# Performance work log

Hardware: AMD Instinct MI355X
Metric: run time of the kernel (lower is better)

Reference implementation:

```python
import jax, jax.numpy as jnp
import numpy as np
import math

H = 512        # hidden_dim
DEPTH = 5
KS = 3         # kernel size
DELTA = 0.1
M = 104        # timestamp == seq_len
NC = 5
B = 512
BN_EPS = 1e-5


def setup_inputs() -> dict:
    key = jax.random.key(0)
    ks = jax.random.split(key, 16)
    inp = {}
    inp['x'] = jax.random.normal(ks[0], (B, 1, M), dtype=jnp.float32)
    # CausalCNN: depth conv layers (first is 1->H, rest H->H), each followed by BN
    inp['conv_w0'] = jax.random.normal(ks[1], (H, 1, KS), dtype=jnp.float32) * (1.0 / np.sqrt(KS))
    inp['conv_b0'] = jnp.zeros((H,), jnp.float32)
    inp['conv_w'] = jax.random.normal(ks[2], (DEPTH - 1, H, H, KS), dtype=jnp.float32) * (1.0 / np.sqrt(H * KS))
    inp['conv_b'] = jnp.zeros((DEPTH - 1, H), jnp.float32)
    inp['bn_gamma'] = jnp.ones((DEPTH, H), jnp.float32)
    inp['bn_beta'] = jnp.zeros((DEPTH, H), jnp.float32)
    # input_proj
    inp['proj_w'] = jax.random.normal(ks[3], (H, H), dtype=jnp.float32) * (1.0 / np.sqrt(H))
    inp['proj_b'] = jnp.zeros((H,), jnp.float32)
    # ZOH layers: A = -0.01*I + 0.001*randn, B = 0.01*randn [H,1], C = 0.01*randn [1,H]
    eye = jnp.eye(H, dtype=jnp.float32)
    inp['A_all'] = -0.01 * eye[None] + 0.001 * jax.random.normal(ks[4], (DEPTH, H, H), dtype=jnp.float32)
    inp['B_all'] = 0.01 * jax.random.normal(ks[5], (DEPTH, H, 1), dtype=jnp.float32)
    inp['C_all'] = 0.01 * jax.random.normal(ks[6], (DEPTH, 1, H), dtype=jnp.float32)
    # fc_temp: Linear(H,H) -> BN1d(H) -> GELU -> Dropout(eval) -> Linear(H,NC)
    inp['fc1_w'] = jax.random.normal(ks[7], (H, H), dtype=jnp.float32) * (1.0 / np.sqrt(H))
    inp['fc1_b'] = jnp.zeros((H,), jnp.float32)
    inp['fc_bn_gamma'] = jnp.ones((H,), jnp.float32)
    inp['fc_bn_beta'] = jnp.zeros((H,), jnp.float32)
    inp['fc2_w'] = jax.random.normal(ks[8], (NC, H), dtype=jnp.float32) * (1.0 / np.sqrt(H))
    inp['fc2_b'] = jnp.zeros((NC,), jnp.float32)
    return inp


def _causal_conv(x, w, b):
    # x: [B, Cin, T], w: [Cout, Cin, K] -> left-pad K-1 (equivalent to pad both + trim right)
    y = jax.lax.conv_general_dilated(x, w, window_strides=(1,), padding=[(KS - 1, 0)],
                                     dimension_numbers=('NCH', 'OIH', 'NCH'))
    return y + b[None, :, None]


def _bn_ct(x, g, b):
    # BatchNorm1d over [B, C, T], batch statistics (training-mode normalization)
    m = x.mean(axis=(0, 2), keepdims=True)
    v = x.var(axis=(0, 2), keepdims=True)
    return g[None, :, None] * (x - m) * jax.lax.rsqrt(v + BN_EPS) + b[None, :, None]


def _pos_encoding(T, d):
    pos = jnp.arange(T, dtype=jnp.float32)[:, None]
    div = jnp.exp(jnp.arange(0, d, 2, dtype=jnp.float32) * (-math.log(10000.0) / d))
    pe = jnp.zeros((T, d), jnp.float32)
    pe = pe.at[:, 0::2].set(jnp.sin(pos * div))
    pe = pe.at[:, 1::2].set(jnp.cos(pos * div))
    return pe


def _zoh_kbar(A, Bv, Cv):
    # A: [H,H], Bv: [H,1], Cv: [1,H] -> normalized K_bar [M]
    A_bar = jax.scipy.linalg.expm(DELTA * A)
    I = jnp.eye(H, dtype=A.dtype)
    A_inv = jnp.linalg.inv(A + 0.001 * I)
    B_bar = A_inv @ (A_bar - I) @ (DELTA * Bv)  # [H,1]
    # term_k = C @ A_bar^k @ B_bar; sequential vector recurrence replaces matrix powers
    def step(v, _):
        term = (Cv @ v)[0, 0]
        return A_bar @ v, term
    _, terms = jax.lax.scan(step, B_bar, None, length=M)  # [M]
    Kb = jnp.flip(terms, axis=0)
    return Kb / (jnp.linalg.norm(Kb) + 1e-6)


def reference(x, conv_w0, conv_b0, conv_w, conv_b, bn_gamma, bn_beta, proj_w, proj_b,
              A_all, B_all, C_all, fc1_w, fc1_b, fc_bn_gamma, fc_bn_beta, fc2_w, fc2_b):
    # CausalCNN
    h = jax.nn.relu(_bn_ct(_causal_conv(x, conv_w0, conv_b0), bn_gamma[0], bn_beta[0]))
    for i in range(DEPTH - 1):
        h = jax.nn.relu(_bn_ct(_causal_conv(h, conv_w[i], conv_b[i]), bn_gamma[i + 1], bn_beta[i + 1]))
    h = jnp.transpose(h, (0, 2, 1))  # [B, T, H]
    # positional encoding + input projection
    h = h + _pos_encoding(M, H)[None]
    h = jnp.einsum('bth,oh->bto', h, proj_w) + proj_b
    # stacked ZOH kernels: each layer multiplies x by its normalized K_bar along time
    Ks = jax.vmap(_zoh_kbar)(A_all, B_all, C_all)  # [DEPTH, M]
    h = h * jnp.prod(Ks, axis=0)[None, :, None]
    # mean pool over time, then fc_temp (BN with batch stats, dropout = identity/eval)
    h = h.mean(axis=1)  # [B, H]
    h = jnp.dot(h, fc1_w.T) + fc1_b
    m = h.mean(axis=0, keepdims=True)
    v = h.var(axis=0, keepdims=True)
    h = fc_bn_gamma * (h - m) * jax.lax.rsqrt(v + BN_EPS) + fc_bn_beta
    h = jax.nn.gelu(h, approximate=False)
    logits = jnp.dot(h, fc2_w.T) + fc2_b  # [B, NC]
    return logits
```

## Files before the change

kernel.cpp:

```cpp
#include <hip/hip_runtime.h>
#include <cstdio>
#include <cmath>
#include <cstdint>

constexpr int BM = 512 * 104;
constexpr float BN_EPS = 1e-5f;

constexpr size_t SZ_BF   = (size_t)BM * 512 * 2;
constexpr size_t SZ_MAT5 = (size_t)5 * 512 * 512 * 4;
constexpr size_t OFF_YB0 = 0;
constexpr size_t OFF_YB1 = OFF_YB0 + SZ_BF;
constexpr size_t OFF_WT2 = OFF_YB1 + SZ_BF;
constexpr size_t OFF_X   = OFF_WT2 + 6291456;
constexpr size_t OFF_T1  = OFF_X   + SZ_MAT5;
constexpr size_t OFF_T2  = OFF_T1  + SZ_MAT5;
constexpr size_t OFF_E   = OFF_T2  + SZ_MAT5;
constexpr size_t OFF_MW  = OFF_E   + SZ_MAT5;
constexpr size_t OFF_P2  = OFF_MW  + SZ_MAT5;
constexpr size_t OFF_P4  = OFF_P2  + SZ_MAT5;
constexpr size_t OFF_ROWT= OFF_P4  + SZ_MAT5;
constexpr size_t OFF_COLS= OFF_ROWT + 655360;
constexpr size_t OFF_COLS2=OFF_COLS + 655360;
constexpr size_t OFF_PIVI= OFF_COLS2 + 655360;
constexpr size_t OFF_PJT = OFF_PIVI + 81920;
// ... 7 lines not shown
constexpr size_t OFF_V   = OFF_SV  + 10240;
constexpr size_t OFF_WV  = OFF_V   + 81920;
constexpr size_t OFF_S   = OFF_WV  + 133120;
constexpr size_t WS_NEED = OFF_S + 512;

__device__ __forceinline__ float bf2f(unsigned short u) {
    union { uint32_t i; float f; } x; x.i = (uint32_t)u << 16; return x.f;
}
__device__ __forceinline__ unsigned short f2bf(float f) {
    union { float f; uint32_t i; } x; x.f = f;
    uint32_t r = x.i + 0x7FFFu + ((x.i >> 16) & 1u);
    return (unsigned short)(r >> 16);
}

typedef __bf16 bf16x8 __attribute__((ext_vector_type(8)));
typedef float  f32x4  __attribute__((ext_vector_type(4)));

__device__ __forceinline__ void gld16(const void* g, void* l) {
    __builtin_amdgcn_global_load_lds((const __attribute__((address_space(1))) uint32_t*)g,
                                     (__attribute__((address_space(3))) uint32_t*)l, 16, 0, 0);
}

__device__ __forceinline__ uint32_t bnrelu_pk(uint32_t u, float sc0, float sc1, float sh0, float sh1) {
    union { uint32_t i; float f; } a, b;
    a.i = u << 16;
    b.i = u & 0xFFFF0000u;
    float x0 = fmaxf(fmaf(a.f, sc0, sh0), 0.0f);
    float x1 = fmaxf(fmaf(b.f, sc1, sh1), 0.0f);
    uint32_t r;
    asm volatile("v_cvt_pk_bf16_f32 %0, %1, %2" : "=v"(r) : "v"(x0), "v"(x1));
    return r;
}

__global__ void k_bw(const float* __restrict__ W, unsigned short* __restrict__ Wt2,
                     const float* __restrict__ Aall, float* __restrict__ X, float* __restrict__ MW,
                     float* __restrict__ COLSa, const float* __restrict__ Call, float* __restrict__ WV)
{
    int bid = blockIdx.x;
    int tid = threadIdx.x;
    if (bid < 2048) {
        int co = bid & 511, l = bid >> 9;
        const float* src = W + (long)(l * 512 + co) * 512 * 3;
        unsigned short* dst = Wt2 + (long)l * 3 * 262144 + ((long)co << 9);
        int v = (co >> 1) & 3;
#pragma unroll
        for (int q = 0; q < 2; ++q) {
            int ci = tid * 2 + q;
            int chunk = (ci >> 3) & 3;
            int di = (ci & ~31) + (((chunk ^ v) & 3) << 3) + (ci & 7);
            float f0 = src[ci * 3 + 0], f1 = src[ci * 3 + 1], f2 = src[ci * 3 + 2];
            dst[di] = f2bf(f0);
            dst[262144 + di] = f2bf(f1);
            dst[524288 + di] = f2bf(f2);
        }
        return;
    }
    long i = (long)(bid - 2048) * 256 + tid;
    float a = Aall[i];
    X[i] = 0.1f * a;
    int z = (int)(i >> 18);
    int rc = (int)(i & 262143);
    int r = rc >> 9, c = rc & 511;
    float mw = a + ((r == c) ? 0.001f : 0.0f);
    MW[i] = mw;
    if (c < 64) COLSa[(long)z * 32768 + r * 64 + c] = mw;
    if (i < 2560) WV[(i >> 9) * 6656 + (i & 511)] = Call[i];
}

__global__ __launch_bounds__(256) void k_mm(
    const float* __restrict__ A, long sA, int lda,
    const float* __restrict__ Bm, long sB, int ldb,
    float* __restrict__ C, long sC, int ldc,
    int K, int mode,
    const float* __restrict__ aux, long sAux,
    const float* __restrict__ aux2, float* __restrict__ Cp,
    double* __restrict__ st1, double* __restrict__ st2, int pc)
{
    __shared__ float sm[2 * 32 * 68];
    float* As = sm;
    float* Bs = sm + 32 * 68;
    int z = blockIdx.z;
    A  += (long)z * sA;
    Bm += (long)z * sB;
    C  += (long)z * sC;
    if (aux) aux += (long)z * sAux;
    int m0 = blockIdx.x * 64, n0 = blockIdx.y * 64;
    int tid = threadIdx.x;
    int tx = tid & 15, ty = tid >> 4;
    float acc[4][4] = {};
    for (int k0 = 0; k0 < K; k0 += 32) {
        __syncthreads();
#pragma unroll
        for (int it = 0; it < 2; ++it) {
            int s = it * 256 + tid;
            int mm = s >> 3, k4 = (s & 7) * 4;
            float4 v = *(const float4*)&A[(long)(m0 + mm) * lda + k0 + k4];
            As[(k4 + 0) * 68 + mm] = v.x;
            As[(k4 + 1) * 68 + mm] = v.y;
            As[(k4 + 2) * 68 + mm] = v.z;
// ... 45 lines not shown
                int col = col0 + j;
                pv[j] = ((row == col) ? 0.5f : 0.0f) + aux[(long)row * 512 + col] * (1.0f / 6.0f)
                        + v[j] * (1.0f / 24.0f);
            }
            *(float4*)&Cp[base] = make_float4(pv[0], pv[1], pv[2], pv[3]);
        } else if (mode == 8) {
            for (int j = 0; j < 4; ++j) {
                v[j] += aux[col0 + j];
                cs1[j] += v[j]; cs2[j] += v[j] * v[j];
            }
        }
        *(float4*)&C[base] = make_float4(v[0], v[1], v[2], v[3]);
    }
    if (mode == 8) {
        __syncthreads();
        float* s1s = sm;
        float* s2s = sm + 1024;
#pragma unroll
        for (int j = 0; j < 4; ++j) {
            s1s[ty * 64 + tx * 4 + j] = cs1[j];
            s2s[ty * 64 + tx * 4 + j] = cs2[j];
        }
        __syncthreads();
        if (tid < 64) {
            double a = 0.0, b = 0.0;
#pragma unroll
            for (int t = 0; t < 16; ++t) { a += s1s[t * 64 + tid]; b += s2s[t * 64 + tid]; }
            atomicAdd(&st1[n0 + tid], a);
            atomicAdd(&st2[n0 + tid], b);
        }
    }
}

__global__ __launch_bounds__(256) void k_elim2(
    const float* __restrict__ MWin, float* __restrict__ MWout,
    const float* __restrict__ PIVI, const float* __restrict__ COLSc,
    float* __restrict__ COLSn, int pc, int pcn)
{
    __shared__ float As[64 * 68];
    __shared__ float Rs[64 * 68];
    int z = blockIdx.z;
    MWin += (long)z * 262144; MWout += (long)z * 262144;
    PIVI += z * 4096; COLSc += (long)z * 32768; COLSn += (long)z * 32768;
    int m0 = blockIdx.x * 64, n0 = blockIdx.y * 64;
    int tid = threadIdx.x;
    int tx = tid & 15, ty = tid >> 4;

    if (n0 == pc) {
        for (int it = 0; it < 16; ++it) {
            int idx = it * 256 + tid;
            int r = idx >> 6, c = idx & 63;
            Rs[r * 68 + c] = PIVI[r * 64 + c];
        }
        __syncthreads();
    } else {
        {
            int m = tid >> 2, kb = (tid & 3) * 16;
#pragma unroll
            for (int u = 0; u < 4; ++u) {
                float4 v = *(const float4*)&PIVI[m * 64 + kb + u * 4];
                As[(kb + u * 4 + 0) * 68 + m] = v.x;
                As[(kb + u * 4 + 1) * 68 + m] = v.y;
                As[(kb + u * 4 + 2) * 68 + m] = v.z;
                As[(kb + u * 4 + 3) * 68 + m] = v.w;
            }
            int kr = tid >> 2, cb = (tid & 3) * 16;
#pragma unroll
            for (int u = 0; u < 4; ++u)
                *(float4*)&Rs[kr * 68 + cb + u * 4] =
                    *(const float4*)&MWin[(long)(pc + kr) * 512 + n0 + cb + u * 4];
        }
        __syncthreads();
        float acc1[4][4] = {};
// ... 24 lines not shown
            int r = idx >> 6, c = idx & 63;
            float v = Rs[r * 68 + c];
            MWout[(long)(pc + r) * 512 + n0 + c] = v;
            if (n0 == pcn) COLSn[(pc + r) * 64 + c] = v;
        }
        return;
    }
    {
        int m = tid >> 2, kb = (tid & 3) * 16;
#pragma unroll
        for (int u = 0; u < 4; ++u) {
            float4 v = *(const float4*)&COLSc[(m0 + m) * 64 + kb + u * 4];
            As[(kb + u * 4 + 0) * 68 + m] = v.x;
            As[(kb + u * 4 + 1) * 68 + m] = v.y;
            As[(kb + u * 4 + 2) * 68 + m] = v.z;
            As[(kb + u * 4 + 3) * 68 + m] = v.w;
        }
    }
    __syncthreads();
    float acc[4][4] = {};
#pragma unroll 8
    for (int kk = 0; kk < 64; ++kk) {
        float4 a = *(const float4*)&As[kk * 68 + ty * 4];
        float4 b = *(const float4*)&Rs[kk * 68 + tx * 4];
        float av[4] = {a.x, a.y, a.z, a.w};
        float bv[4] = {b.x, b.y, b.z, b.w};
#pragma unroll
        for (int i = 0; i < 4; ++i)
#pragma unroll
            for (int j = 0; j < 4; ++j)
                acc[i][j] = fmaf(av[i], bv[j], acc[i][j]);
    }
    bool inP = (n0 == pc);
#pragma unroll
    for (int i = 0; i < 4; ++i) {
        int row = m0 + ty * 4 + i;
        int col0 = n0 + tx * 4;
        long base = (long)row * 512 + col0;
        float ov[4] = {0.f, 0.f, 0.f, 0.f};
        if (!inP) {
            float4 oldv = *(const float4*)&MWin[base];
            ov[0] = oldv.x; ov[1] = oldv.y; ov[2] = oldv.z; ov[3] = oldv.w;
        }
        float v[4];
#pragma unroll
        for (int j = 0; j < 4; ++j) v[j] = ov[j] - acc[i][j];
        *(float4*)&MWout[base] = make_float4(v[0], v[1], v[2], v[3]);
        if (n0 == pcn)
            *(float4*)&COLSn[row * 64 + (col0 - pcn)] = make_float4(v[0], v[1], v[2], v[3]);
    }
}

__global__ __launch_bounds__(256) void k_inv64(const float* __restrict__ MW, int pblk, float* __restrict__ PIVI)
{
    __shared__ float mat[64 * 65];
    __shared__ float fv[64];
    __shared__ int perm[64];
    __shared__ int arr[64];
    __shared__ int pividx;
    __shared__ float dv;
    int z = blockIdx.x;
    const float* Mg = MW + (long)z * 262144 + (long)pblk * 64 * 512 + pblk * 64;
    int tid = threadIdx.x;
    for (int it = 0; it < 16; ++it) {
        int idx = it * 256 + tid;
        int r = idx >> 6, c = idx & 63;
        mat[r * 65 + c] = Mg[r * 512 + c];
    }
    __syncthreads();
    for (int j = 0; j < 64; ++j) {
        if (tid < 64) {
            float v = (tid >= j) ? fabsf(mat[tid * 65 + j]) : -1.0f;
            int idx = tid;
#pragma unroll
            for (int off = 32; off; off >>= 1) {
                float ov = __shfl_down(v, off);
                int oi = __shfl_down(idx, off);
                if (ov > v) { v = ov; idx = oi; }
            }
            if (tid == 0) pividx = idx;
        }
        __syncthreads();
// ... 13 lines not shown
            mat[j * 65 + tid] = (tid == j) ? d : mat[j * 65 + tid] * d;
            if (tid == 0) dv = d;
        }
        __syncthreads();
        {
            int i = tid & 63, c0 = (tid >> 6) * 16;
            if (i != j) {
                float f = fv[i];
                float dd = dv;
#pragma unroll
                for (int u = 0; u < 16; ++u) {
                    int c = c0 + u;
                    float val = mat[i * 65 + c] - f * mat[j * 65 + c];
                    if (c == j) val = -f * dd;
                    mat[i * 65 + c] = val;
                }
            }
        }
        __syncthreads();
    }
    if (tid == 0) {
        for (int c = 0; c < 64; ++c) arr[c] = c;
        for (int j = 63; j >= 0; --j) { int r = perm[j]; int t = arr[j]; arr[j] = arr[r]; arr[r] = t; }
    }
    __syncthreads();
    float* Pg = PIVI + z * 4096;
    for (int it = 0; it < 16; ++it) {
        int idx = it * 256 + tid;
        int r = idx >> 6, c = idx & 63;
        Pg[r * 64 + c] = mat[r * 65 + arr[c]];
    }
}

__global__ __launch_bounds__(1024) void k_bbar(const float* __restrict__ Eb, const float* __restrict__ MW,
                                               const float* __restrict__ Aall, const float* __restrict__ Ball,
                                               float* __restrict__ V)
{
    __shared__ float xs[512], us[512], vs[512], sv[512];
    int z = blockIdx.x;
    const float* E  = Eb   + (long)z * 262144;
    const float* Mi = MW   + (long)z * 262144;
    const float* Aa = Aall + (long)z * 262144;
    int tid = threadIdx.x, lane = tid & 63, w = tid >> 6;
    if (tid < 512) xs[tid] = Ball[z * 512 + tid];
    __syncthreads();
    for (int r = w * 32; r < w * 32 + 32; ++r) {
        const float* ar = E + (long)r * 512;
        double acc = 0.0;
#pragma unroll
        for (int m = 0; m < 8; ++m) acc += (double)ar[lane + m * 64] * (double)xs[lane + m * 64];
        for (int off = 32; off; off >>= 1) acc += __shfl_down(acc, off);
        if (lane == 0) us[r] = 0.1f * (float)acc;
    }
    __syncthreads();
    for (int r = w * 32; r < w * 32 + 32; ++r) {
        const float* ar = Mi + (long)r * 512;
        double acc = 0.0;
#pragma unroll
        for (int m = 0; m < 8; ++m) acc += (double)ar[lane + m * 64] * (double)us[lane + m * 64];
        for (int off = 32; off; off >>= 1) acc += __shfl_down(acc, off);
        if (lane == 0) vs[r] = 1.0f * (float)acc;
    }
    __syncthreads();
    for (int r = w * 32; r < w * 32 + 32; ++r) {
        const float* ar = Aa + (long)r * 512;
        double acc = 0.0;
#pragma unroll
        for (int m = 0; m < 8; ++m) acc += (double)ar[lane + m * 64] * (double)vs[lane + m * 64];
        for (int off = 32; off; off >>= 1) acc += __shfl_down(acc, off);
        if (lane == 0) {
            float val = 1.0f * (float)acc + 0.001f * vs[r];
            sv[r] = us[r] - val;
        }
    }
    __syncthreads();
    for (int r = w * 32; r < w * 32 + 32; ++r) {
        const float* ar = Mi + (long)r * 512;
        double acc = 0.0;
#pragma unroll
        for (int m = 0; m < 8; ++m) acc += (double)ar[lane + m * 64] * (double)sv[lane + m * 64];
        for (int off = 32; off; off >>= 1) acc += __shfl_down(acc, off);
        if (lane == 0) V[(long)z * 4096 + r] = vs[r] + 1.0f * (float)acc;
    }
}

struct VWT { long a[8]; long x[8]; long y[8]; float al[8]; float be[8]; int ty[8]; };
__global__ void k_vw(const char* __restrict__ ws, VWT T)
{
    int g = blockIdx.x, z = blockIdx.y, t = blockIdx.z;
    int lane = threadIdx.x;
    const float* A = (const float*)(ws + T.a[t]) + (long)z * 262144;
    int ty = T.ty[t];
    long vs = ty ? 6656 : 4096;
    const float* x = (const float*)(ws + T.x[t]) + (long)z * vs;
    float* yv = (float*)(ws + T.y[t]) + (long)z * vs;
    if (ty == 0) {
        float xm[8];
#pragma unroll
        for (int m = 0; m < 8; ++m) xm[m] = x[lane + m * 64];
        float alpha = T.al[t], beta = T.be[t];
        for (int r0 = 0; r0 < 64; ++r0) {
            int row = g * 64 + r0;
            const float* ar = A + (long)row * 512;
            double acc = 0.0;
#pragma unroll
            for (int m = 0; m < 8; ++m) acc += (double)ar[lane + m * 64] * (double)xm[m];
            for (int off = 32; off; off >>= 1) acc += __shfl_down(acc, off);
            if (lane == 0) yv[row] = alpha * (float)acc + beta * x[row];
        }
    } else {
        __shared__ float xl[512];
#pragma unroll
        for (int m = 0; m < 8; ++m) xl[lane + m * 64] = x[lane + m * 64];
        __syncthreads();
        int c = g * 64 + lane;
        double acc = 0.0;
#pragma unroll 8
        for (int j = 0; j < 512; ++j) acc += (double)A[(long)j * 512 + c] * (double)xl[j];
        yv[c] = (float)acc;
    }
}

__global__ __launch_bounds__(512) void k_termsk(const float* __restrict__ WV, const float* __restrict__ V,
                                                float* __restrict__ svec)
{
    __shared__ float tl[520];
    __shared__ float invn[5];
    __shared__ float red[2];
    int tid = threadIdx.x;
    for (int t = tid; t < 520; t += 512) {
        int z = t / 104, d = t - z * 104;
        int j = d >> 3, i = d & 7;
        const float* wp = WV + z * 6656 + j * 512;
        const float* vp = V + z * 4096 + i * 512;
        float acc = 0.0f;
#pragma unroll 8
        for (int k = 0; k < 512; ++k) acc += wp[k] * vp[k];
        tl[t] = acc;
    }
    __syncthreads();
    int w = tid >> 6, lane = tid & 63;
    if (w < 5) {
        float a = tl[w * 104 + lane]; a = a * a;
        if (lane < 40) { float b = tl[w * 104 + 64 + lane]; a += b * b; }
#pragma unroll
        for (int off = 32; off; off >>= 1) a += __shfl_down(a, off);
        if (lane == 0) invn[w] = 1.0f / (sqrtf(a) + 1e-6f);
    }
    __syncthreads();
    float s = 0.0f;
    if (tid < 104) {
        s = 1.0f;
        for (int l = 0; l < 5; ++l) s *= tl[l * 104 + (103 - tid)] * invn[l];
        svec[tid] = s;
    }
    if (tid < 128) {
        float v = (tid < 104) ? s : 0.0f;
#pragma unroll
        for (int off = 32; off; off >>= 1) v += __shfl_down(v, off);
        if ((tid & 63) == 0) red[tid >> 6] = v;
    }
    __syncthreads();
    if (tid == 0) svec[104] = (red[0] + red[1]) * (1.0f / 104.0f);
}

__global__ void k_conv0(const float* __restrict__ x, const float* __restrict__ w0, const float* __restrict__ b0,
                        unsigned short* __restrict__ y, double* __restrict__ s1g, double* __restrict__ s2g)
{
    int b = blockIdx.x;
    int c = blockIdx.y * 256 + threadIdx.x;
    float w_0 = w0[c * 3 + 0], w_1 = w0[c * 3 + 1], w_2 = w0[c * 3 + 2], bb = b0[c];
    const float* xb = x + b * 104;
    unsigned short* yb = y + (long)b * 104 * 512 + c;
    float xm2 = 0.0f, xm1 = 0.0f;
    float s1 = 0.0f, s2 = 0.0f;
    for (int t = 0; t < 104; ++t) {
        float x0 = xb[t];
        float v = w_0 * xm2 + w_1 * xm1 + w_2 * x0 + bb;
        yb[t * 512] = f2bf(v);
        s1 += v; s2 += v * v;
        xm2 = xm1; xm1 = x0;
    }
    atomicAdd(&s1g[c], (double)s1);
    atomicAdd(&s2g[c], (double)s2);
}

__global__ __launch_bounds__(256, 2) void k_convm(
    const unsigned short* __restrict__ act,
    const unsigned short* __restrict__ Wt2,
    const float* __restrict__ bias,
    const double* __restrict__ STin,
    const float* __restrict__ gam, const float* __restrict__ bet,
    unsigned short* __restrict__ yout,
    double* __restrict__ s1g, double* __restrict__ s2g)
{
    __shared__ __align__(16) unsigned short As[130 * 32];
    __shared__ __align__(16) unsigned short Bs[3 * 256 * 32];
    __shared__ float SCs[512];
    __shared__ float SHs[512];
    int tid = threadIdx.x;
    int m0 = blockIdx.x * 128, co0 = blockIdx.y * 256;
    int w = tid >> 6, lane = tid & 63;
    int wr = (w >> 1) * 64, wc = (w & 1) * 128;
    int fr = lane & 15, quad = lane >> 4;

    const double invN = 1.0 / (double)BM;
    for (int c = tid; c < 512; c += 256) {
        double mn = STin[c] * invN;
        double var = STin[512 + c] * invN - mn * mn;
        double rs = 1.0 / sqrt(var + (double)BN_EPS);
        double scd = (double)gam[c] * rs;
        SCs[c] = (float)scd;
        SHs[c] = (float)((double)bet[c] - mn * scd);
    }

    bool valid[4][3];
#pragma unroll
    for (int i = 0; i < 4; ++i) {
        int R = m0 + wr + i * 16 + fr;
        int t = R % 104;
#pragma unroll
        for (int tau = 0; tau < 3; ++tau) valid[i][tau] = (t + tau >= 2);
    }

    int aoff[4][3];
#pragma unroll
    for (int i = 0; i < 4; ++i)
#pragma unroll
        for (int tau = 0; tau < 3; ++tau) {
            int r = wr + i * 16 + fr + tau;
            aoff[i][tau] = r * 32 + (((quad ^ (r >> 1)) & 3) << 3);
        }
    int boff[8];
// ... 118 lines not shown
        float b = st[512 + half * 128 + cl] + st[512 + (half + 2) * 128 + cl];
        atomicAdd(&s1g[co0 + tid], (double)a);
        atomicAdd(&s2g[co0 + tid], (double)b);
    }
}

__global__ void k_pool(const unsigned short* __restrict__ y4, const double* __restrict__ ST4,
                       const float* __restrict__ gam, const float* __restrict__ bet,
                       const float* __restrict__ svec, float* __restrict__ g)
{
    __shared__ float sl[104];
    int b = blockIdx.x;
    int c = blockIdx.y * 256 + threadIdx.x;
    if (threadIdx.x < 104) sl[threadIdx.x] = svec[threadIdx.x];
    __syncthreads();
    const double invN = 1.0 / (double)BM;
    double mn = ST4[c] * invN;
    double var = ST4[512 + c] * invN - mn * mn;
    double rs = 1.0 / sqrt(var + (double)BN_EPS);
    double scd = (double)gam[c] * rs;
    float sc = (float)scd, sh = (float)((double)bet[c] - mn * scd);
    int he = c & ~1;
    float div = expf((float)he * (-0.017988946039015984f));
    float acc = 0.0f;
    const unsigned short* yb = y4 + (long)b * 104 * 512 + c;
    for (int t = 0; t < 104; ++t) {
        float v = bf2f(yb[t * 512]);
        float hn = fmaxf(fmaf(v, sc, sh), 0.0f);
        float arg = (float)t * div;
        float pe = (c & 1) ? cosf(arg) : sinf(arg);
        acc += sl[t] * (hn + pe);
    }
    g[(long)b * 512 + c] = acc * (1.0f / 104.0f);
}

__global__ void k_t512(const float* __restrict__ in0, float* __restrict__ out0,
                       const float* __restrict__ in1, float* __restrict__ out1)
{
    __shared__ float tile[64 * 68];
    const float* in = blockIdx.z ? in1 : in0;
    float* outp = blockIdx.z ? out1 : out0;
    int bx = blockIdx.x, by = blockIdx.y;
    int tid = threadIdx.x;
    for (int it = 0; it < 4; ++it) {
        int s = it * 256 + tid;
        int r = s >> 4, c4 = (s & 15) * 4;
        *(float4*)&tile[r * 68 + c4] = *(const float4*)&in[(long)(bx * 64 + r) * 512 + by * 64 + c4];
    }
    __syncthreads();
    for (int it = 0; it < 4; ++it) {
        int s = it * 256 + tid;
        int r = s >> 4, c4 = (s & 15) * 4;
        float4 v;
        v.x = tile[(c4 + 0) * 68 + r];
        v.y = tile[(c4 + 1) * 68 + r];
        v.z = tile[(c4 + 2) * 68 + r];
        v.w = tile[(c4 + 3) * 68 + r];
        *(float4*)&outp[(long)(by * 64 + r) * 512 + bx * 64 + c4] = v;
    }
}

__global__ __launch_bounds__(256) void k_final(const float* __restrict__ zin, const double* __restrict__ st,
                                               const float* __restrict__ gam, const float* __restrict__ bet,
                                               const float* __restrict__ w2, const float* __restrict__ b2,
                                               float* __restrict__ outp)
{
    __shared__ float red[256];
    int b = blockIdx.x, tid = threadIdx.x;
    int oo[2] = { tid, tid + 256 };
    float gv[2];
#pragma unroll
    for (int q = 0; q < 2; ++q) {
        int o = oo[q];
        double m = st[o] * (1.0 / 512.0);
        double var = st[512 + o] * (1.0 / 512.0) - m * m;
        double rs = 1.0 / sqrt(var + (double)BN_EPS);
        float xn = (float)(((double)zin[(long)b * 512 + o] - m) * rs * (double)gam[o] + (double)bet[o]);
        gv[q] = 0.5f * xn * (1.0f + erff(xn * 0.70710678118654752f));
    }
    for (int n = 0; n < 5; ++n) {
        float p = gv[0] * w2[n * 512 + oo[0]] + gv[1] * w2[n * 512 + oo[1]];
        red[tid] = p;
        __syncthreads();
        for (int off = 128; off; off >>= 1) { if (tid < off) red[tid] += red[tid + off]; __syncthreads(); }
        if (tid == 0) outp[b * 5 + n] = red[0] + b2[n];
        __syncthreads();
    }
}

static void mm(hipStream_t s, int Mt, int Nt, int z,
               const float* A, long sA, int lda,
               const float* B, long sB, int ldb,
// ... 15 lines not shown
    const float* conv_w0 = (const float*)d_in[1];
    const float* conv_b0 = (const float*)d_in[2];
    const float* conv_w  = (const float*)d_in[3];
    const float* conv_b  = (const float*)d_in[4];
    const float* bn_g    = (const float*)d_in[5];
    const float* bn_b    = (const float*)d_in[6];
    const float* proj_w  = (const float*)d_in[7];
    const float* proj_b  = (const float*)d_in[8];
    const float* A_all   = (const float*)d_in[9];
    const float* B_all   = (const float*)d_in[10];
    const float* C_all   = (const float*)d_in[11];
    const float* fc1_w   = (const float*)d_in[12];
    const float* fc1_b   = (const float*)d_in[13];
    const float* fbn_g   = (const float*)d_in[14];
    const float* fbn_b   = (const float*)d_in[15];
    const float* fc2_w   = (const float*)d_in[16];
    const float* fc2_b   = (const float*)d_in[17];
    float* outp = (float*)d_out;
    char* ws = (char*)d_ws;
    if (ws_size < WS_NEED) { printf("ws too small: %zu < %zu\n", ws_size, WS_NEED); return; }

    unsigned short* YB0 = (unsigned short*)(ws + OFF_YB0);
    unsigned short* YB1 = (unsigned short*)(ws + OFF_YB1);
    unsigned short* WT2 = (unsigned short*)(ws + OFF_WT2);
    float* Xb   = (float*)(ws + OFF_X);
    float* T1   = (float*)(ws + OFF_T1);
    float* T2   = (float*)(ws + OFF_T2);
    float* Eb   = (float*)(ws + OFF_E);
    float* MW   = (float*)(ws + OFF_MW);
    float* P2   = (float*)(ws + OFF_P2);
    float* P4   = (float*)(ws + OFF_P4);
    float* COLS1= (float*)(ws + OFF_COLS);
    float* COLS2= (float*)(ws + OFF_COLS2);
    float* PIVI = (float*)(ws + OFF_PIVI);
    float* PJT  = (float*)(ws + OFF_PJT);
    float* F1T  = (float*)(ws + OFF_F1T);
    float* G    = (float*)(ws + OFF_G);
    float* POOL = (float*)(ws + OFF_POOL);
    float* Zb   = (float*)(ws + OFF_Z);
    double* ST  = (double*)(ws + OFF_ST);
    float* V    = (float*)(ws + OFF_V);
    float* WV   = (float*)(ws + OFF_WV);
    float* SVEC = (float*)(ws + OFF_S);

    const long SM = 262144;
    hipMemsetAsync(ws + OFF_ST, 0, 49152, stream);

    k_bw<<<7168, 256, 0, stream>>>(conv_w, WT2, A_all, Xb, MW, COLS1, C_all, WV);

    {
        float* MB[2] = { MW, P2 };
        for (int p = 0; p < 8; ++p) {
            int pc = p * 64;
            float* Mi = MB[p & 1];
            float* Mo = MB[(p + 1) & 1];
            float* Cc = (p & 1) ? COLS2 : COLS1;
            float* Cn = (p & 1) ? COLS1 : COLS2;
            k_inv64<<<5, 256, 0, stream>>>(Mi, p, PIVI);
            k_elim2<<<dim3(8, 8, 5), 256, 0, stream>>>(Mi, Mo, PIVI, Cc, Cn, pc, pc + 64);
        }
    }
    mm(stream, 8, 8, 5, Xb, SM, 512, Xb, SM, 512, T2, SM, 512, 512, 7, Xb, SM, nullptr, T1);
    mm(stream, 8, 8, 5, T2, SM, 512, T1, SM, 512, Eb, SM, 512, 512, 2, Xb, SM);
    mm(stream, 8, 8, 5, Eb, SM, 512, Eb, SM, 512, Xb, SM, 512, 512, 1, Eb, SM);
    mm(stream, 8, 8, 5, Xb, SM, 512, Xb, SM, 512, T1, SM, 512, 512, 0);
    mm(stream, 8, 8, 5, T1, SM, 512, T1, SM, 512, T2, SM, 512, 512, 0);
    mm(stream, 8, 8, 5, T2, SM, 512, T2, SM, 512, P2, SM, 512, 512, 0);
    mm(stream, 8, 8, 5, P2, SM, 512, P2, SM, 512, P4, SM, 512, 512, 0);
    k_bbar<<<5, 1024, 0, stream>>>(Eb, MW, A_all, B_all, V);
    auto Voff = [](int i) { return (long)(OFF_V + (size_t)i * 2048); };
    auto Woff = [](int j) { return (long)(OFF_WV + (size_t)j * 2048); };
    {
        VWT T = {};
        T.a[0] = OFF_E;  T.x[0] = Voff(0); T.y[0] = Voff(1); T.al[0] = 1; T.be[0] = 1; T.ty[0] = 0;
        T.a[1] = OFF_T2; T.x[1] = Woff(0); T.y[1] = Woff(1); T.ty[1] = 1;
        k_vw<<<dim3(8, 5, 2), 64, 0, stream>>>(ws, T);
    }
    {
        VWT T = {};
        T.a[0] = OFF_X;  T.x[0] = Voff(0); T.y[0] = Voff(2); T.al[0] = 1; T.ty[0] = 0;
        T.a[1] = OFF_X;  T.x[1] = Voff(1); T.y[1] = Voff(3); T.al[1] = 1; T.ty[1] = 0;
        T.a[2] = OFF_P2; T.x[2] = Woff(0); T.y[2] = Woff(2); T.ty[2] = 1;
        T.a[3] = OFF_P2; T.x[3] = Woff(1); T.y[3] = Woff(3); T.ty[3] = 1;
        k_vw<<<dim3(8, 5, 4), 64, 0, stream>>>(ws, T);
    }
    {
        VWT T = {};
        for (int i = 0; i < 4; ++i) {
            T.a[i] = OFF_T1; T.x[i] = Voff(i); T.y[i] = Voff(4 + i); T.al[i] = 1; T.ty[i] = 0;
            T.a[4 + i] = OFF_P4; T.x[4 + i] = Woff(i); T.y[4 + i] = Woff(4 + i); T.ty[4 + i] = 1;
        }
        k_vw<<<dim3(8, 5, 8), 64, 0, stream>>>(ws, T);
    }
    {
        VWT T = {};
        for (int i = 0; i < 4; ++i) {
            T.a[i] = OFF_P4; T.x[i] = Woff(4 + i); T.y[i] = Woff(8 + i); T.ty[i] = 1;
        }
        k_vw<<<dim3(8, 5, 4), 64, 0, stream>>>(ws, T);
    }
    {
        VWT T = {};
        T.a[0] = OFF_P4; T.x[0] = Woff(8); T.y[0] = Woff(12); T.ty[0] = 1;
        k_vw<<<dim3(8, 5, 1), 64, 0, stream>>>(ws, T);
    }
    k_termsk<<<1, 512, 0, stream>>>(WV, V, SVEC);

    k_conv0<<<dim3(512, 2), 256, 0, stream>>>(x, conv_w0, conv_b0, YB0, ST, ST + 512);
    for (int l = 1; l <= 4; ++l) {
        unsigned short* inb  = (l & 1) ? YB0 : YB1;
        unsigned short* outb = (l & 1) ? YB1 : YB0;
        k_convm<<<dim3(416, 2), 256, 0, stream>>>(inb, WT2 + (size_t)(l - 1) * 3 * 262144,
                                                  conv_b + (l - 1) * 512,
                                                  ST + (l - 1) * 1024, bn_g + (l - 1) * 512, bn_b + (l - 1) * 512,
                                                  outb, ST + l * 1024, ST + l * 1024 + 512);
    }
    k_pool<<<dim3(512, 2), 256, 0, stream>>>(YB0, ST + 4 * 1024, bn_g + 4 * 512, bn_b + 4 * 512, SVEC, G);

    k_t512<<<dim3(8, 8, 2), 256, 0, stream>>>(proj_w, PJT, fc1_w, F1T);
    mm(stream, 8, 8, 1, G, 0, 512, PJT, 0, 512, POOL, 0, 512, 512, 5, proj_b, 0, SVEC + 104);
    mm(stream, 8, 8, 1, POOL, 0, 512, F1T, 0, 512, Zb, 0, 512, 512, 8, fc1_b, 0, nullptr, nullptr,
       ST + 5 * 1024, ST + 5 * 1024 + 512);
    k_final<<<512, 256, 0, stream>>>(Zb, ST + 5 * 1024, fbn_g, fbn_b, fc2_w, fc2_b, outp);
}
```

Before: 1.834 ms.

## Fuse small launches: pre-pass, pivot inversion into elimination, ZOH vector chain

Several small kernels are merged. The weight transposes and the first conv layer now run inside one pre-pass kernel. The 64x64 pivot-block inversion for the next step is folded into the elimination kernel, so only one block per batch does it. The chain of matrix-vector kernels plus k_bbar becomes one k_zoh kernel, and the k_termsk reduction rides on an extra block of the first conv layer. The goal is to cut launch overhead and serial small-kernel gaps. In exchange, the work is concentrated in a few blocks: the inversion tail of the elimination and five 1024-thread ZOH blocks, which may serialize.

```diff
diff --git a/kernel.cpp b/kernel.cpp
--- a/kernel.cpp
+++ b/kernel.cpp
@@ -63,10 +63,16 @@
     return r;
 }
 
-__global__ void k_bw(const float* __restrict__ W, unsigned short* __restrict__ Wt2,
-                     const float* __restrict__ Aall, float* __restrict__ X, float* __restrict__ MW,
-                     float* __restrict__ COLSa, const float* __restrict__ Call, float* __restrict__ WV)
+__global__ void k_pre(const float* __restrict__ W, unsigned short* __restrict__ Wt2,
+                      const float* __restrict__ Aall, float* __restrict__ X, float* __restrict__ MW,
+                      float* __restrict__ COLSa, const float* __restrict__ Call, float* __restrict__ WV,
+                      const float* __restrict__ pin0, float* __restrict__ pout0,
+                      const float* __restrict__ pin1, float* __restrict__ pout1,
+                      const float* __restrict__ xin, const float* __restrict__ w0,
+                      const float* __restrict__ b0, unsigned short* __restrict__ y0,
+                      double* __restrict__ s1g, double* __restrict__ s2g)
 {
+    __shared__ float tile[64 * 68];
     int bid = blockIdx.x;
     int tid = threadIdx.x;
     if (bid < 2048) {
@@ -86,16 +92,61 @@
         }
         return;
     }
-    long i = (long)(bid - 2048) * 256 + tid;
-    float a = Aall[i];
-    X[i] = 0.1f * a;
-    int z = (int)(i >> 18);
-    int rc = (int)(i & 262143);
-    int r = rc >> 9, c = rc & 511;
-    float mw = a + ((r == c) ? 0.001f : 0.0f);
-    MW[i] = mw;
-    if (c < 64) COLSa[(long)z * 32768 + r * 64 + c] = mw;
-    if (i < 2560) WV[(i >> 9) * 6656 + (i & 511)] = Call[i];
+    if (bid < 7168) {
+        long i = (long)(bid - 2048) * 256 + tid;
+        float a = Aall[i];
+        X[i] = 0.1f * a;
+        int z = (int)(i >> 18);
+        int rc = (int)(i & 262143);
+        int r = rc >> 9, c = rc & 511;
+        float mw = a + ((r == c) ? 0.001f : 0.0f);
+        MW[i] = mw;
+        if (c < 64) COLSa[(long)z * 32768 + r * 64 + c] = mw;
+        if (i < 2560) WV[(i >> 9) * 6656 + (i & 511)] = Call[i];
+        return;
+    }
+    if (bid < 7296) {
+        int id = bid - 7168;
+        int bx = id & 7, by = (id >> 3) & 7, zi = id >> 6;
+        const float* in = zi ? pin1 : pin0;
+        float* outp = zi ? pout1 : pout0;
+        for (int it = 0; it < 4; ++it) {
+            int s = it * 256 + tid;
+            int r = s >> 4, c4 = (s & 15) * 4;
+            *(float4*)&tile[r * 68 + c4] = *(const float4*)&in[(long)(bx * 64 + r) * 512 + by * 64 + c4];
+        }
+        __syncthreads();
+        for (int it = 0; it < 4; ++it) {
+            int s = it * 256 + tid;
+            int r = s >> 4, c4 = (s & 15) * 4;
+            float4 v;
+            v.x = tile[(c4 + 0) * 68 + r];
+            v.y = tile[(c4 + 1) * 68 + r];
+            v.z = tile[(c4 + 2) * 68 + r];
+            v.w = tile[(c4 + 3) * 68 + r];
+            *(float4*)&outp[(long)(by * 64 + r) * 512 + bx * 64 + c4] = v;
+        }
+        return;
+    }
+    {
+        int id = bid - 7296;
+        int b = id & 511;
+        int c = (id >> 9) * 256 + tid;
+        float w_0 = w0[c * 3 + 0], w_1 = w0[c * 3 + 1], w_2 = w0[c * 3 + 2], bb = b0[c];
+        const float* xb = xin + b * 104;
+        unsigned short* yb = y0 + (long)b * 104 * 512 + c;
+        float xm2 = 0.0f, xm1 = 0.0f;
+        float s1 = 0.0f, s2 = 0.0f;
+        for (int t = 0; t < 104; ++t) {
+            float x0 = xb[t];
+            float v = w_0 * xm2 + w_1 * xm1 + w_2 * x0 + bb;
+            yb[t * 512] = f2bf(v);
+            s1 += v; s2 += v * v;
+            xm2 = xm1; xm1 = x0;
+        }
+        atomicAdd(&s1g[c], (double)s1);
+        atomicAdd(&s2g[c], (double)s2);
+    }
 }
 
 __global__ __launch_bounds__(256) void k_mm(
@@ -207,13 +258,18 @@
     }
 }
 
-__global__ __launch_bounds__(256) void k_elim2(
+__global__ __launch_bounds__(256) void k_elim3(
     const float* __restrict__ MWin, float* __restrict__ MWout,
-    const float* __restrict__ PIVI, const float* __restrict__ COLSc,
-    float* __restrict__ COLSn, int pc, int pcn)
+    const float* __restrict__ PIVI, float* __restrict__ PIVN,
+    const float* __restrict__ COLSc, float* __restrict__ COLSn, int pc, int pcn)
 {
     __shared__ float As[64 * 68];
     __shared__ float Rs[64 * 68];
+    __shared__ float fv[64];
+    __shared__ int perm[64];
+    __shared__ int arr[64];
+    __shared__ int pividx;
+    __shared__ float dv;
     int z = blockIdx.z;
     MWin += (long)z * 262144; MWout += (long)z * 262144;
     PIVI += z * 4096; COLSc += (long)z * 32768; COLSn += (long)z * 32768;
@@ -304,6 +360,7 @@
                 acc[i][j] = fmaf(av[i], bv[j], acc[i][j]);
     }
     bool inP = (n0 == pc);
+    float vsav[4][4];
 #pragma unroll
     for (int i = 0; i < 4; ++i) {
         int row = m0 + ty * 4 + i;
@@ -316,10 +373,77 @@
         }
         float v[4];
 #pragma unroll
-        for (int j = 0; j < 4; ++j) v[j] = ov[j] - acc[i][j];
+        for (int j = 0; j < 4; ++j) { v[j] = ov[j] - acc[i][j]; vsav[i][j] = v[j]; }
         *(float4*)&MWout[base] = make_float4(v[0], v[1], v[2], v[3]);
         if (n0 == pcn)
             *(float4*)&COLSn[row * 64 + (col0 - pcn)] = make_float4(v[0], v[1], v[2], v[3]);
+    }
+
+    if (!(m0 == pcn && n0 == pcn)) return;
+    __syncthreads();
+    float* mat = As;
+#pragma unroll
+    for (int i = 0; i < 4; ++i)
+#pragma unroll
+        for (int j = 0; j < 4; ++j)
+            mat[(ty * 4 + i) * 65 + tx * 4 + j] = vsav[i][j];
+    __syncthreads();
+    for (int j = 0; j < 64; ++j) {
+        if (tid < 64) {
+            float v = (tid >= j) ? fabsf(mat[tid * 65 + j]) : -1.0f;
+            int idx = tid;
+#pragma unroll
+            for (int off = 32; off; off >>= 1) {
+                float ov = __shfl_down(v, off);
+                int oi = __shfl_down(idx, off);
+                if (ov > v) { v = ov; idx = oi; }
+            }
+            if (tid == 0) pividx = idx;
+        }
+        __syncthreads();
+        int r = pividx;
+        if (tid < 64) {
+            if (r != j) {
+                float tj = mat[j * 65 + tid], tr = mat[r * 65 + tid];
+                mat[j * 65 + tid] = tr; mat[r * 65 + tid] = tj;
+            }
+            if (tid == 0) perm[j] = r;
+        }
+        __syncthreads();
+        if (tid < 64) {
+            float piv = mat[j * 65 + j];
+            float d = 1.0f / piv;
+            fv[tid] = mat[tid * 65 + j];
+            mat[j * 65 + tid] = (tid == j) ? d : mat[j * 65 + tid] * d;
+            if (tid == 0) dv = d;
+        }
+        __syncthreads();
+        {
+            int i = tid & 63, c0 = (tid >> 6) * 16;
+            if (i != j) {
+                float f = fv[i];
+                float dd = dv;
+#pragma unroll
+                for (int u = 0; u < 16; ++u) {
+                    int c = c0 + u;
+                    float val = mat[i * 65 + c] - f * mat[j * 65 + c];
+                    if (c == j) val = -f * dd;
+                    mat[i * 65 + c] = val;
+                }
+            }
+        }
+        __syncthreads();
+    }
+    if (tid == 0) {
+        for (int c = 0; c < 64; ++c) arr[c] = c;
+        for (int j = 63; j >= 0; --j) { int r = perm[j]; int t = arr[j]; arr[j] = arr[r]; arr[r] = t; }
+    }
+    __syncthreads();
+    float* Pg = PIVN + z * 4096;
+    for (int it = 0; it < 16; ++it) {
+        int idx = it * 256 + tid;
+        int r = idx >> 6, c = idx & 63;
+        Pg[r * 64 + c] = mat[r * 65 + arr[c]];
     }
 }
 
@@ -399,17 +523,26 @@
     }
 }
 
-__global__ __launch_bounds__(1024) void k_bbar(const float* __restrict__ Eb, const float* __restrict__ MW,
-                                               const float* __restrict__ Aall, const float* __restrict__ Ball,
-                                               float* __restrict__ V)
+__global__ __launch_bounds__(1024) void k_zoh(const char* __restrict__ ws,
+                                              const float* __restrict__ Aall,
+                                              const float* __restrict__ Ball)
 {
-    __shared__ float xs[512], us[512], vs[512], sv[512];
+    __shared__ float Vs[8][512];
+    __shared__ float Ws[13][512];
+    __shared__ float xs[512], us[512], sv[512];
     int z = blockIdx.x;
-    const float* E  = Eb   + (long)z * 262144;
-    const float* Mi = MW   + (long)z * 262144;
-    const float* Aa = Aall + (long)z * 262144;
+    const float* E   = (const float*)(ws + OFF_E)  + (long)z * 262144;
+    const float* A2p = (const float*)(ws + OFF_X)  + (long)z * 262144;
+    const float* A4p = (const float*)(ws + OFF_T1) + (long)z * 262144;
+    const float* A8p = (const float*)(ws + OFF_T2) + (long)z * 262144;
+    const float* A16p= (const float*)(ws + OFF_P2) + (long)z * 262144;
+    const float* A32p= (const float*)(ws + OFF_P4) + (long)z * 262144;
+    const float* Mi  = (const float*)(ws + OFF_MW) + (long)z * 262144;
+    const float* Aa  = Aall + (long)z * 262144;
+    float* Vg = (float*)(ws + OFF_V)  + (long)z * 4096;
+    float* Wg = (float*)(ws + OFF_WV) + (long)z * 6656;
     int tid = threadIdx.x, lane = tid & 63, w = tid >> 6;
-    if (tid < 512) xs[tid] = Ball[z * 512 + tid];
+    if (tid < 512) { xs[tid] = Ball[z * 512 + tid]; Ws[0][tid] = Wg[tid]; }
     __syncthreads();
     for (int r = w * 32; r < w * 32 + 32; ++r) {
         const float* ar = E + (long)r * 512;
@@ -426,17 +559,17 @@
 #pragma unroll
         for (int m = 0; m < 8; ++m) acc += (double)ar[lane + m * 64] * (double)us[lane + m * 64];
         for (int off = 32; off; off >>= 1) acc += __shfl_down(acc, off);
-        if (lane == 0) vs[r] = 1.0f * (float)acc;
+        if (lane == 0) Vs[0][r] = 1.0f * (float)acc;
     }
     __syncthreads();
     for (int r = w * 32; r < w * 32 + 32; ++r) {
         const float* ar = Aa + (long)r * 512;
         double acc = 0.0;
 #pragma unroll
-        for (int m = 0; m < 8; ++m) acc += (double)ar[lane + m * 64] * (double)vs[lane + m * 64];
+        for (int m = 0; m < 8; ++m) acc += (double)ar[lane + m * 64] * (double)Vs[0][lane + m * 64];
         for (int off = 32; off; off >>= 1) acc += __shfl_down(acc, off);
         if (lane == 0) {
-            float val = 1.0f * (float)acc + 0.001f * vs[r];
+            float val = 1.0f * (float)acc + 0.001f * Vs[0][r];
             sv[r] = us[r] - val;
         }
     }
@@ -447,109 +580,103 @@
 #pragma unroll
         for (int m = 0; m < 8; ++m) acc += (double)ar[lane + m * 64] * (double)sv[lane + m * 64];
         for (int off = 32; off; off >>= 1) acc += __shfl_down(acc, off);
-        if (lane == 0) V[(long)z * 4096 + r] = vs[r] + 1.0f * (float)acc;
-    }
-}
-
-struct VWT { long a[8]; long x[8]; long y[8]; float al[8]; float be[8]; int ty[8]; };
-__global__ void k_vw(const char* __restrict__ ws, VWT T)
-{
-    int g = blockIdx.x, z = blockIdx.y, t = blockIdx.z;
-    int lane = threadIdx.x;
-    const float* A = (const float*)(ws + T.a[t]) + (long)z * 262144;
-    int ty = T.ty[t];
-    long vs = ty ? 6656 : 4096;
-    const float* x = (const float*)(ws + T.x[t]) + (long)z * vs;
-    float* yv = (float*)(ws + T.y[t]) + (long)z * vs;
-    if (ty == 0) {
+        if (lane == 0) Vs[0][r] = Vs[0][r] + 1.0f * (float)acc;
+    }
+    __syncthreads();
+    if (w < 8) {
         float xm[8];
 #pragma unroll
-        for (int m = 0; m < 8; ++m) xm[m] = x[lane + m * 64];
-        float alpha = T.al[t], beta = T.be[t];
-        for (int r0 = 0; r0 < 64; ++r0) {
-            int row = g * 64 + r0;
-            const float* ar = A + (long)row * 512;
+        for (int m = 0; m < 8; ++m) xm[m] = Vs[0][lane + m * 64];
+        for (int r = w * 64; r < w * 64 + 64; ++r) {
+            const float* ar = E + (long)r * 512;
             double acc = 0.0;
 #pragma unroll
             for (int m = 0; m < 8; ++m) acc += (double)ar[lane + m * 64] * (double)xm[m];
             for (int off = 32; off; off >>= 1) acc += __shfl_down(acc, off);
-            if (lane == 0) yv[row] = alpha * (float)acc + beta * x[row];
+            if (lane == 0) Vs[1][r] = 1.0f * (float)acc + 1.0f * Vs[0][r];
         }
     } else {
-        __shared__ float xl[512];
-#pragma unroll
-        for (int m = 0; m < 8; ++m) xl[lane + m * 64] = x[lane + m * 64];
-        __syncthreads();
-        int c = g * 64 + lane;
+        int c = tid - 512;
         double acc = 0.0;
 #pragma unroll 8
-        for (int j = 0; j < 512; ++j) acc += (double)A[(long)j * 512 + c] * (double)xl[j];
-        yv[c] = (float)acc;
-    }
-}
-
-__global__ __launch_bounds__(512) void k_termsk(const float* __restrict__ WV, const float* __restrict__ V,
-                                                float* __restrict__ svec)
-{
-    __shared__ float tl[520];
-    __shared__ float invn[5];
-    __shared__ float red[2];
-    int tid = threadIdx.x;
-    for (int t = tid; t < 520; t += 512) {
-        int z = t / 104, d = t - z * 104;
-        int j = d >> 3, i = d & 7;
-        const float* wp = WV + z * 6656 + j * 512;
-        const float* vp = V + z * 4096 + i * 512;
-        float acc = 0.0f;
+        for (int j = 0; j < 512; ++j) acc += (double)A8p[(long)j * 512 + c] * (double)Ws[0][j];
+        Ws[1][c] = (float)acc;
+    }
+    __syncthreads();
+    if (w < 8) {
+        const float* xv = (w < 4) ? Vs[0] : Vs[1];
+        float* yv = (w < 4) ? Vs[2] : Vs[3];
+        int r0 = (w & 3) * 128;
+        float xm[8];
+#pragma unroll
+        for (int m = 0; m < 8; ++m) xm[m] = xv[lane + m * 64];
+        for (int r = r0; r < r0 + 128; ++r) {
+            const float* ar = A2p + (long)r * 512;
+            double acc = 0.0;
+#pragma unroll
+            for (int m = 0; m < 8; ++m) acc += (double)ar[lane + m * 64] * (double)xm[m];
+            for (int off = 32; off; off >>= 1) acc += __shfl_down(acc, off);
+            if (lane == 0) yv[r] = (float)acc;
+        }
+    } else {
+        const float* xv = (w < 12) ? Ws[0] : Ws[1];
+        float* yv = (w < 12) ? Ws[2] : Ws[3];
+        int q = (w < 12) ? (tid - 512) : (tid - 768);
+        for (int u = 0; u < 2; ++u) {
+            int c = q + u * 256;
+            double acc = 0.0;
 #pragma unroll 8
-        for (int k = 0; k < 512; ++k) acc += wp[k] * vp[k];
-        tl[t] = acc;
-    }
-    __syncthreads();
-    int w = tid >> 6, lane = tid & 63;
-    if (w < 5) {
-        float a = tl[w * 104 + lane]; a = a * a;
-        if (lane < 40) { float b = tl[w * 104 + 64 + lane]; a += b * b; }
-#pragma unroll
-        for (int off = 32; off; off >>= 1) a += __shfl_down(a, off);
-        if (lane == 0) invn[w] = 1.0f / (sqrtf(a) + 1e-6f);
-    }
-    __syncthreads();
-    float s = 0.0f;
-    if (tid < 104) {
-        s = 1.0f;
-        for (int l = 0; l < 5; ++l) s *= tl[l * 104 + (103 - tid)] * invn[l];
-        svec[tid] = s;
-    }
-    if (tid < 128) {
-        float v = (tid < 104) ? s : 0.0f;
-#pragma unroll
-        for (int off = 32; off; off >>= 1) v += __shfl_down(v, off);
-        if ((tid & 63) == 0) red[tid >> 6] = v;
-    }
-    __syncthreads();
-    if (tid == 0) svec[104] = (red[0] + red[1]) * (1.0f / 104.0f);
-}
-
-__global__ void k_conv0(const float* __restrict__ x, const float* __restrict__ w0, const float* __restrict__ b0,
-                        unsigned short* __restrict__ y, double* __restrict__ s1g, double* __restrict__ s2g)
-{
-    int b = blockIdx.x;
-    int c = blockIdx.y * 256 + threadIdx.x;
-    float w_0 = w0[c * 3 + 0], w_1 = w0[c * 3 + 1], w_2 = w0[c * 3 + 2], bb = b0[c];
-    const float* xb = x + b * 104;
-    unsigned short* yb = y + (long)b * 104 * 512 + c;
-    float xm2 = 0.0f, xm1 = 0.0f;
-    float s1 = 0.0f, s2 = 0.0f;
-    for (int t = 0; t < 104; ++t) {
-        float x0 = xb[t];
-        float v = w_0 * xm2 + w_1 * xm1 + w_2 * x0 + bb;
-        yb[t * 512] = f2bf(v);
-        s1 += v; s2 += v * v;
-        xm2 = xm1; xm1 = x0;
-    }
-    atomicAdd(&s1g[c], (double)s1);
-    atomicAdd(&s2g[c], (double)s2);
+            for (int j = 0; j < 512; ++j) acc += (double)A16p[(long)j * 512 + c] * (double)xv[j];
+            yv[c] = (float)acc;
+        }
+    }
+    __syncthreads();
+    if (w < 8) {
+        int t = w >> 1, r0 = (w & 1) * 256;
+        float xm[8];
+#pragma unroll
+        for (int m = 0; m < 8; ++m) xm[m] = Vs[t][lane + m * 64];
+        for (int r = r0; r < r0 + 256; ++r) {
+            const float* ar = A4p + (long)r * 512;
+            double acc = 0.0;
+#pragma unroll
+            for (int m = 0; m < 8; ++m) acc += (double)ar[lane + m * 64] * (double)xm[m];
+            for (int off = 32; off; off >>= 1) acc += __shfl_down(acc, off);
+            if (lane == 0) Vs[4 + t][r] = (float)acc;
+        }
+    } else {
+        int c = tid - 512;
+        double a0 = 0.0, a1 = 0.0, a2 = 0.0, a3 = 0.0;
+#pragma unroll 8
+        for (int j = 0; j < 512; ++j) {
+            double a = (double)A32p[(long)j * 512 + c];
+            a0 += a * (double)Ws[0][j]; a1 += a * (double)Ws[1][j];
+            a2 += a * (double)Ws[2][j]; a3 += a * (double)Ws[3][j];
+        }
+        Ws[4][c] = (float)a0; Ws[5][c] = (float)a1; Ws[6][c] = (float)a2; Ws[7][c] = (float)a3;
+    }
+    __syncthreads();
+    if (tid < 512) {
+        int c = tid;
+        double a0 = 0.0, a1 = 0.0, a2 = 0.0, a3 = 0.0;
+#pragma unroll 8
+        for (int j = 0; j < 512; ++j) {
+            double a = (double)A32p[(long)j * 512 + c];
+            a0 += a * (double)Ws[4][j]; a1 += a * (double)Ws[5][j];
+            a2 += a * (double)Ws[6][j]; a3 += a * (double)Ws[7][j];
+        }
+        Ws[8][c] = (float)a0; Ws[9][c] = (float)a1; Ws[10][c] = (float)a2; Ws[11][c] = (float)a3;
+    }
+    __syncthreads();
+    if (tid < 512) {
+        double acc = 0.0;
+#pragma unroll 8
+        for (int j = 0; j < 512; ++j) acc += (double)A32p[(long)j * 512 + tid] * (double)Ws[8][j];
+        Ws[12][tid] = (float)acc;
+    }
+    __syncthreads();
+    for (int idx = tid; idx < 8 * 512; idx += 1024) Vg[idx] = ((float*)Vs)[idx];
+    for (int idx = tid; idx < 13 * 512; idx += 1024) Wg[idx] = ((float*)Ws)[idx];
 }
 
 __global__ __launch_bounds__(256, 2) void k_convm(
@@ -559,13 +686,55 @@
     const double* __restrict__ STin,
     const float* __restrict__ gam, const float* __restrict__ bet,
     unsigned short* __restrict__ yout,
-    double* __restrict__ s1g, double* __restrict__ s2g)
+    double* __restrict__ s1g, double* __restrict__ s2g,
+    const float* __restrict__ WVt, const float* __restrict__ Vt, float* __restrict__ SVECt)
 {
     __shared__ __align__(16) unsigned short As[130 * 32];
     __shared__ __align__(16) unsigned short Bs[3 * 256 * 32];
     __shared__ float SCs[512];
     __shared__ float SHs[512];
+    __shared__ float invk[5];
+    __shared__ float redk[2];
     int tid = threadIdx.x;
+    if (blockIdx.x == 416) {
+        if (blockIdx.y != 0 || WVt == nullptr) return;
+        float* tl = (float*)As;
+        for (int t = tid; t < 520; t += 256) {
+            int z = t / 104, d = t - z * 104;
+            int j = d >> 3, i = d & 7;
+            const float* wp = WVt + z * 6656 + j * 512;
+            const float* vp = Vt + z * 4096 + i * 512;
+            float acc = 0.0f;
+#pragma unroll 8
+            for (int k = 0; k < 512; ++k) acc += wp[k] * vp[k];
+            tl[t] = acc;
+        }
+        __syncthreads();
+        int lane = tid & 63;
+        for (int g = tid >> 6; g < 5; g += 4) {
+            float a = tl[g * 104 + lane]; a = a * a;
+            if (lane < 40) { float b = tl[g * 104 + 64 + lane]; a += b * b; }
+#pragma unroll
+            for (int off = 32; off; off >>= 1) a += __shfl_down(a, off);
+            if (lane == 0) invk[g] = 1.0f / (sqrtf(a) + 1e-6f);
+        }
+        __syncthreads();
+        float s = 0.0f;
+        if (tid < 104) {
+            s = 1.0f;
+            for (int l = 0; l < 5; ++l) s *= tl[l * 104 + (103 - tid)] * invk[l];
+            SVECt[tid] = s;
+        }
+        if (tid < 128) {
+            float v = (tid < 104) ? s : 0.0f;
+#pragma unroll
+            for (int off = 32; off; off >>= 1) v += __shfl_down(v, off);
+            if ((tid & 63) == 0) redk[tid >> 6] = v;
+        }
+        __syncthreads();
+        if (tid == 0) SVECt[104] = (redk[0] + redk[1]) * (1.0f / 104.0f);
+        return;
+    }
     int m0 = blockIdx.x * 128, co0 = blockIdx.y * 256;
     int w = tid >> 6, lane = tid & 63;
     int wr = (w >> 1) * 64, wc = (w & 1) * 128;
@@ -750,32 +919,6 @@
         acc += sl[t] * (hn + pe);
     }
     g[(long)b * 512 + c] = acc * (1.0f / 104.0f);
-}
-
-__global__ void k_t512(const float* __restrict__ in0, float* __restrict__ out0,
-                       const float* __restrict__ in1, float* __restrict__ out1)
-{
-    __shared__ float tile[64 * 68];
-    const float* in = blockIdx.z ? in1 : in0;
-    float* outp = blockIdx.z ? out1 : out0;
-    int bx = blockIdx.x, by = blockIdx.y;
-    int tid = threadIdx.x;
-    for (int it = 0; it < 4; ++it) {
-        int s = it * 256 + tid;
-        int r = s >> 4, c4 = (s & 15) * 4;
-        *(float4*)&tile[r * 68 + c4] = *(const float4*)&in[(long)(bx * 64 + r) * 512 + by * 64 + c4];
-    }
-    __syncthreads();
-    for (int it = 0; it < 4; ++it) {
-        int s = it * 256 + tid;
-        int r = s >> 4, c4 = (s & 15) * 4;
-        float4 v;
-        v.x = tile[(c4 + 0) * 68 + r];
-        v.y = tile[(c4 + 1) * 68 + r];
-        v.z = tile[(c4 + 2) * 68 + r];
-        v.w = tile[(c4 + 3) * 68 + r];
-        *(float4*)&outp[(long)(by * 64 + r) * 512 + bx * 64 + c4] = v;
-    }
 }
 
 __global__ __launch_bounds__(256) void k_final(const float* __restrict__ zin, const double* __restrict__ st,
@@ -857,7 +1000,8 @@
     float* P4   = (float*)(ws + OFF_P4);
     float* COLS1= (float*)(ws + OFF_COLS);
     float* COLS2= (float*)(ws + OFF_COLS2);
-    float* PIVI = (float*)(ws + OFF_PIVI);
+    float* PIVA = (float*)(ws + OFF_PIVI);
+    float* PIVB = (float*)(ws + OFF_ROWT);
     float* PJT  = (float*)(ws + OFF_PJT);
     float* F1T  = (float*)(ws + OFF_F1T);
     float* G    = (float*)(ws + OFF_G);
@@ -871,18 +1015,21 @@
     const long SM = 262144;
     hipMemsetAsync(ws + OFF_ST, 0, 49152, stream);
 
-    k_bw<<<7168, 256, 0, stream>>>(conv_w, WT2, A_all, Xb, MW, COLS1, C_all, WV);
+    k_pre<<<8320, 256, 0, stream>>>(conv_w, WT2, A_all, Xb, MW, COLS1, C_all, WV,
+                                    proj_w, PJT, fc1_w, F1T,
+                                    x, conv_w0, conv_b0, YB0, ST, ST + 512);
 
     {
-        float* MB[2] = { MW, P2 };
+        float* MB[2]  = { MW, P2 };
+        float* PB[2]  = { PIVA, PIVB };
+        k_inv64<<<5, 256, 0, stream>>>(MW, 0, PB[0]);
         for (int p = 0; p < 8; ++p) {
             int pc = p * 64;
-            float* Mi = MB[p & 1];
-            float* Mo = MB[(p + 1) & 1];
             float* Cc = (p & 1) ? COLS2 : COLS1;
             float* Cn = (p & 1) ? COLS1 : COLS2;
-            k_inv64<<<5, 256, 0, stream>>>(Mi, p, PIVI);
-            k_elim2<<<dim3(8, 8, 5), 256, 0, stream>>>(Mi, Mo, PIVI, Cc, Cn, pc, pc + 64);
+            k_elim3<<<dim3(8, 8, 5), 256, 0, stream>>>(MB[p & 1], MB[(p + 1) & 1],
+                                                       PB[p & 1], PB[(p + 1) & 1],
+                                                       Cc, Cn, pc, pc + 64);
         }
     }
     mm(stream, 8, 8, 5, Xb, SM, 512, Xb, SM, 512, T2, SM, 512, 512, 7, Xb, SM, nullptr, T1);
@@ -892,57 +1039,20 @@
     mm(stream, 8, 8, 5, T1, SM, 512, T1, SM, 512, T2, SM, 512, 512, 0);
     mm(stream, 8, 8, 5, T2, SM, 512, T2, SM, 512, P2, SM, 512, 512, 0);
     mm(stream, 8, 8, 5, P2, SM, 512, P2, SM, 512, P4, SM, 512, 512, 0);
-    k_bbar<<<5, 1024, 0, stream>>>(Eb, MW, A_all, B_all, V);
-    auto Voff = [](int i) { return (long)(OFF_V + (size_t)i * 2048); };
-    auto Woff = [](int j) { return (long)(OFF_WV + (size_t)j * 2048); };
-    {
-        VWT T = {};
-        T.a[0] = OFF_E;  T.x[0] = Voff(0); T.y[0] = Voff(1); T.al[0] = 1; T.be[0] = 1; T.ty[0] = 0;
-        T.a[1] = OFF_T2; T.x[1] = Woff(0); T.y[1] = Woff(1); T.ty[1] = 1;
-        k_vw<<<dim3(8, 5, 2), 64, 0, stream>>>(ws, T);
-    }
-    {
-        VWT T = {};
-        T.a[0] = OFF_X;  T.x[0] = Voff(0); T.y[0] = Voff(2); T.al[0] = 1; T.ty[0] = 0;
-        T.a[1] = OFF_X;  T.x[1] = Voff(1); T.y[1] = Voff(3); T.al[1] = 1; T.ty[1] = 0;
-        T.a[2] = OFF_P2; T.x[2] = Woff(0); T.y[2] = Woff(2); T.ty[2] = 1;
-        T.a[3] = OFF_P2; T.x[3] = Woff(1); T.y[3] = Woff(3); T.ty[3] = 1;
-        k_vw<<<dim3(8, 5, 4), 64, 0, stream>>>(ws, T);
-    }
-    {
-        VWT T = {};
-        for (int i = 0; i < 4; ++i) {
-            T.a[i] = OFF_T1; T.x[i] = Voff(i); T.y[i] = Voff(4 + i); T.al[i] = 1; T.ty[i] = 0;
-            T.a[4 + i] = OFF_P4; T.x[4 + i] = Woff(i); T.y[4 + i] = Woff(4 + i); T.ty[4 + i] = 1;
-        }
-        k_vw<<<dim3(8, 5, 8), 64, 0, stream>>>(ws, T);
-    }
-    {
-        VWT T = {};
-        for (int i = 0; i < 4; ++i) {
-            T.a[i] = OFF_P4; T.x[i] = Woff(4 + i); T.y[i] = Woff(8 + i); T.ty[i] = 1;
-        }
-        k_vw<<<dim3(8, 5, 4), 64, 0, stream>>>(ws, T);
-    }
-    {
-        VWT T = {};
-        T.a[0] = OFF_P4; T.x[0] = Woff(8); T.y[0] = Woff(12); T.ty[0] = 1;
-        k_vw<<<dim3(8, 5, 1), 64, 0, stream>>>(ws, T);
-    }
-    k_termsk<<<1, 512, 0, stream>>>(WV, V, SVEC);
-
-    k_conv0<<<dim3(512, 2), 256, 0, stream>>>(x, conv_w0, conv_b0, YB0, ST, ST + 512);
+    k_zoh<<<5, 1024, 0, stream>>>(ws, A_all, B_all);
+
     for (int l = 1; l <= 4; ++l) {
         unsigned short* inb  = (l & 1) ? YB0 : YB1;
         unsigned short* outb = (l & 1) ? YB1 : YB0;
-        k_convm<<<dim3(416, 2), 256, 0, stream>>>(inb, WT2 + (size_t)(l - 1) * 3 * 262144,
-                                                  conv_b + (l - 1) * 512,
-                                                  ST + (l - 1) * 1024, bn_g + (l - 1) * 512, bn_b + (l - 1) * 512,
-                                                  outb, ST + l * 1024, ST + l * 1024 + 512);
+        dim3 grid(l == 1 ? 417 : 416, 2);
+        k_convm<<<grid, 256, 0, stream>>>(inb, WT2 + (size_t)(l - 1) * 3 * 262144,
+                                          conv_b + (l - 1) * 512,
+                                          ST + (l - 1) * 1024, bn_g + (l - 1) * 512, bn_b + (l - 1) * 512,
+                                          outb, ST + l * 1024, ST + l * 1024 + 512,
+                                          (l == 1) ? WV : nullptr, V, SVEC);
     }
     k_pool<<<dim3(512, 2), 256, 0, stream>>>(YB0, ST + 4 * 1024, bn_g + 4 * 512, bn_b + 4 * 512, SVEC, G);
 
-    k_t512<<<dim3(8, 8, 2), 256, 0, stream>>>(proj_w, PJT, fc1_w, F1T);
     mm(stream, 8, 8, 1, G, 0, 512, PJT, 0, 512, POOL, 0, 512, 512, 5, proj_b, 0, SVEC + 104);
     mm(stream, 8, 8, 1, POOL, 0, 512, F1T, 0, 512, Zb, 0, 512, 512, 8, fc1_b, 0, nullptr, nullptr,
        ST + 5 * 1024, ST + 5 * 1024 + 512);
```

Measured after the change: 1.964 ms. 1.07x slower.
